# Kernel optimization log

Hardware: AMD Instinct MI355X
Metric: run time of the kernel (lower is better)

Reference implementation:

```python
import jax, jax.numpy as jnp
import numpy as np

B, Ng, C, H, W, Nt, M, P = 4, 8192, 256, 128, 128, 512, 8, 4
Ch = C // M  # 32 channels per head
EPS = 1e-5


def setup_inputs():
    key = jax.random.key(0)
    ks = jax.random.split(key, 12)
    s = 0.02
    def w(k, shape):
        return jax.random.normal(k, shape, jnp.float32) * s
    return {
        "query": jax.random.normal(ks[0], (B, Ng, C), jnp.float32),
        "value": jax.random.normal(ks[1], (B, C, H, W), jnp.float32),
        "reference_points": jax.random.uniform(ks[2], (B, Ng, 2), dtype=jnp.float32),
        "trajectory_points": jax.random.uniform(ks[3], (B, Nt, 2), dtype=jnp.float32),
        "in_proj_w": w(ks[4], (3 * C, C)),
        "in_proj_b": jnp.zeros((3 * C,), jnp.float32),
        "mha_out_w": w(ks[5], (C, C)),
        "mha_out_b": jnp.zeros((C,), jnp.float32),
        "ln_g": jnp.ones((C,), jnp.float32),
        "ln_b": jnp.zeros((C,), jnp.float32),
        "traj_w": w(ks[6], (C, 2)),
        "traj_b": jnp.zeros((C,), jnp.float32),
        "offs_w": w(ks[7], (M * P * 2, C)),
        "offs_b": jnp.zeros((M * P * 2,), jnp.float32),
        "attw_w": w(ks[8], (M * P, C)),
        "attw_b": jnp.zeros((M * P,), jnp.float32),
        "out_w": w(ks[9], (C, C)),
        "out_b": jnp.zeros((C,), jnp.float32),
    }


def _bilinear_sample(imgf, x, y):
    # imgf: (NM, Ch, H*W); x, y: (NM, Lq, P) unnormalized pixel coords
    # grid_sample semantics: bilinear, padding_mode='zeros', align_corners=False
    NM = imgf.shape[0]
    Lq, Pp = x.shape[1], x.shape[2]
    x0 = jnp.floor(x); y0 = jnp.floor(y)
    x1 = x0 + 1.0;     y1 = y0 + 1.0

    def gather(xi, yi):
        valid = (xi >= 0) & (xi < W) & (yi >= 0) & (yi < H)
        xc = jnp.clip(xi, 0, W - 1).astype(jnp.int32)
        yc = jnp.clip(yi, 0, H - 1).astype(jnp.int32)
        idx = (yc * W + xc).reshape(NM, 1, Lq * Pp)
        v = jnp.take_along_axis(imgf, jnp.broadcast_to(idx, (NM, Ch, Lq * Pp)), axis=2)
        return v.reshape(NM, Ch, Lq, Pp), valid.astype(imgf.dtype)

    v00, m00 = gather(x0, y0)
    v01, m01 = gather(x1, y0)
    v10, m10 = gather(x0, y1)
    v11, m11 = gather(x1, y1)
    wx1 = x - x0; wx0 = 1.0 - wx1
    wy1 = y - y0; wy0 = 1.0 - wy1
    out = (v00 * (wx0 * wy0 * m00)[:, None]
         + v01 * (wx1 * wy0 * m01)[:, None]
         + v10 * (wx0 * wy1 * m10)[:, None]
         + v11 * (wx1 * wy1 * m11)[:, None])
    return out  # (NM, Ch, Lq, P)


def reference(query, value, reference_points, trajectory_points,
              in_proj_w, in_proj_b, mha_out_w, mha_out_b, ln_g, ln_b,
              traj_w, traj_b, offs_w, offs_b, attw_w, attw_b, out_w, out_b):
    # trajectory projection: (B,Nt,2) -> (B,Nt,C)
    tf = trajectory_points @ traj_w.T + traj_b

    # guidance cross-attention (nn.MultiheadAttention, eval mode => no dropout)
    wq, wk, wv = jnp.split(in_proj_w, 3, axis=0)
    bq, bk, bv = jnp.split(in_proj_b, 3, axis=0)
    q = (query @ wq.T + bq).reshape(B, Ng, M, Ch)
    k = (tf @ wk.T + bk).reshape(B, Nt, M, Ch)
    v = (tf @ wv.T + bv).reshape(B, Nt, M, Ch)
    scores = jnp.einsum('bqmc,bkmc->bmqk', q, k) / jnp.sqrt(jnp.float32(Ch))
    probs = jax.nn.softmax(scores, axis=-1)
    ctx = jnp.einsum('bmqk,bkmc->bqmc', probs, v).reshape(B, Ng, C)
    ctx = ctx @ mha_out_w.T + mha_out_b

    # residual + LayerNorm
    x = query + ctx
    mu = x.mean(-1, keepdims=True)
    var = ((x - mu) ** 2).mean(-1, keepdims=True)
    gq = (x - mu) / jnp.sqrt(var + EPS) * ln_g + ln_b

    # sampling offsets & softmax attention weights (L=1 level)
    offs = (gq @ offs_w.T + offs_b).reshape(B, Ng, M, 1, P, 2)
    aw = jax.nn.softmax((gq @ attw_w.T + attw_b).reshape(B, Ng, M, P), axis=-1)
    loc = reference_points[:, :, None, None, None, :] + offs  # (B,Ng,M,1,P,2)

    # deformable sampling core (single level)
    grid = 2.0 * loc[:, :, :, 0] - 1.0                   # (B,Ng,M,P,2)
    grid = grid.transpose(0, 2, 1, 3, 4).reshape(B * M, Ng, P, 2)
    gx = (grid[..., 0] + 1.0) * (W * 0.5) - 0.5
    gy = (grid[..., 1] + 1.0) * (H * 0.5) - 0.5
    imgf = value.reshape(B * M, Ch, H * W)               # per-head feature maps
    samp = _bilinear_sample(imgf, gx, gy)                # (B*M,Ch,Ng,P)
    w_att = aw.transpose(0, 2, 1, 3).reshape(B * M, 1, Ng, P)
    out = (samp * w_att).sum(-1)                         # (B*M,Ch,Ng)

    # faithful to source: view(B,M,Ch,Ng).transpose(1,2).contiguous().view(B,Ng,C)
    out = out.reshape(B, M, Ch, Ng).transpose(0, 2, 1, 3).reshape(B, Ng, C)
    return out @ out_w.T + out_b
```

## Files before the change

### kernel.cpp

```cpp
#include <hip/hip_runtime.h>
#include <hip/hip_bf16.h>
#include <stdint.h>

typedef __bf16 bf16_t;
typedef __bf16 bf16x8 __attribute__((ext_vector_type(8)));
typedef __bf16 bf16x4 __attribute__((ext_vector_type(4)));
typedef float f32x4 __attribute__((ext_vector_type(4)));

#define CEXP 0.25506807186679906f

__device__ __forceinline__ float ldf(const void* p, size_t i, int isf) {
  return isf ? ((const float*)p)[i] : (float)((const bf16_t*)p)[i];
}

__device__ __forceinline__ int detect_isf(const void* q) {
  const uint16_t* u = (const uint16_t*)q;
  const int lane = threadIdx.x & 63;
  const uint16_t v = u[2 * lane];
  const int e = (v >> 7) & 0xFF;
  const int weird = (e >= 0x86 || (v != 0 && e <= 0x65)) ? 1 : 0;
  return (__popcll(__ballot(weird)) >= 16) ? 1 : 0;
}

__device__ __forceinline__ float fexp2(float x) {
#if __has_builtin(__builtin_amdgcn_exp2f)
  return __builtin_amdgcn_exp2f(x);
#else
  return exp2f(x);
#endif
}

__device__ __forceinline__ f32x4 mfma16x16x16(bf16x4 a, bf16x4 b, f32x4 c) {
#if __has_builtin(__builtin_amdgcn_mfma_f32_16x16x16_bf16)
  return __builtin_amdgcn_mfma_f32_16x16x16_bf16(a, b, c, 0, 0, 0);
#else
  typedef short s16x4 __attribute__((ext_vector_type(4)));
  return __builtin_amdgcn_mfma_f32_16x16x16bf16_1k(
      __builtin_bit_cast(s16x4, a), __builtin_bit_cast(s16x4, b), c, 0, 0, 0);
#endif
}

__device__ __forceinline__ void stage16(const bf16_t* g, bf16_t* l) {
  __builtin_amdgcn_global_load_lds((const __attribute__((address_space(1))) void*)g,
                                   (__attribute__((address_space(3))) void*)l, 16, 0, 0);
}

__global__ __launch_bounds__(256) void prep_all(
    const void* __restrict__ query,
    const void* in_w, const void* in_b, const void* mow, const void* mob,
    const void* outw, const void* outb,
    const void* trajp, const void* tw, const void* tb,
    const void* offs_w, const void* attw_w, const void* offs_b, const void* attw_b,
    bf16_t* __restrict__ blob, bf16_t* __restrict__ tf,
    bf16_t* __restrict__ Wph, bf16_t* __restrict__ Wpl, bf16_t* __restrict__ bp)
{
  const int isf = detect_isf(query);
  const int bid = blockIdx.x;
  if (bid < 322) {
    const int g = (bid * 256 + threadIdx.x) * 4;
    if (g >= 328960) return;
    const void* src; size_t off;
    if      (g < 196608) { src = in_w; off = g; }
    else if (g < 197376) { src = in_b; off = g - 196608; }
    else if (g < 262912) { src = mow;  off = g - 197376; }
    else if (g < 263168) { src = mob;  off = g - 262912; }
    else if (g < 328704) { src = outw; off = g - 263168; }
    else                 { src = outb; off = g - 328704; }
#pragma unroll
    for (int k = 0; k < 4; k++) blob[g + k] = (bf16_t)ldf(src, off + k, isf);
  } else if (bid < 322 + 2048) {
    const int rowb = bid - 322;
    const int c = threadIdx.x;
    const float x = ldf(trajp, rowb * 2 + 0, isf);
    const float y = ldf(trajp, rowb * 2 + 1, isf);
    const float v = x * ldf(tw, c * 2 + 0, isf) + y * ldf(tw, c * 2 + 1, isf) + ldf(tb, c, isf);
    tf[(size_t)rowb * 256 + c] = (bf16_t)v;
  } else {
    const int idx = (bid - 2370) * 256 + threadIdx.x;
    const int rowp = idx >> 8, c = idx & 255;
    float v = 0.0f;
    if (rowp < 64)      v = ldf(offs_w, rowp * 256 + c, isf);
    else if (rowp < 96) v = ldf(attw_w, (rowp - 64) * 256 + c, isf);
    const bf16_t hi = (bf16_t)v;
    Wph[idx] = hi;
    Wpl[idx] = (bf16_t)(v - (float)hi);
    if (idx < 128) {
      float bv = 0.0f;
      if (idx < 64)      bv = ldf(offs_b, idx, isf);
      else if (idx < 96) bv = ldf(attw_b, idx - 64, isf);
      bp[idx] = (bf16_t)bv;
    }
  }
}

#define TM 128
#define TN 128
#define TKK 64

__global__ __launch_bounds__(256) void gemm_async(
    const bf16_t* __restrict__ A, const bf16_t* __restrict__ W,
    const bf16_t* __restrict__ bias, void* __restrict__ Cout,
    void* __restrict__ Cout2, int Ndim, int Kdim, int mode, float kscale,
    const void* __restrict__ qdet)
{
  __shared__ __align__(16) bf16_t As[TM * TKK];
  __shared__ __align__(16) bf16_t Ws[TN * TKK];
  const int t    = threadIdx.x;
  const int lane = t & 63;
  const int w    = t >> 6;
  const int wm   = (w & 1) * 64;
  const int wn   = (w >> 1) * 64;
  const int q4   = lane >> 4;
  const int r16  = lane & 15;
  const int tm   = blockIdx.x * TM;
  const int tn   = blockIdx.y * TN;

  f32x4 acc[4][4] = {};

  for (int kt = 0; kt < Kdim; kt += TKK) {
    __syncthreads();
#pragma unroll
    for (int r = 0; r < 4; r++) {
      const int L = w * 256 + r * 64 + lane;
      const int R = L >> 3, c = (L & 7) * 8;
      stage16(A + (size_t)(tm + R) * Kdim + kt + c, As + L * 8);
      stage16(W + (size_t)(tn + R) * Kdim + kt + c, Ws + L * 8);
    }
    __syncthreads();
#pragma unroll
    for (int ks = 0; ks < TKK; ks += 32) {
      bf16x8 af[4], bfm[4];
#pragma unroll
      for (int i = 0; i < 4; i++)
        af[i] = *(const bf16x8*)(As + (wm + 16 * i + r16) * TKK + ks + q4 * 8);
#pragma unroll
      for (int j = 0; j < 4; j++)
        bfm[j] = *(const bf16x8*)(Ws + (wn + 16 * j + r16) * TKK + ks + q4 * 8);
#pragma unroll
      for (int i = 0; i < 4; i++)
#pragma unroll
        for (int j = 0; j < 4; j++)
          acc[i][j] = __builtin_amdgcn_mfma_f32_16x16x32_bf16(af[i], bfm[j], acc[i][j], 0, 0, 0);
    }
  }

  const int isf = (mode == 3) ? detect_isf(qdet) : 1;
#pragma unroll
  for (int j = 0; j < 4; j++) {
    const int col = tn + wn + 16 * j + r16;
    const float bv = (float)bias[col];
#pragma unroll
    for (int i = 0; i < 4; i++) {
      const int row0 = tm + wm + 16 * i + q4 * 4;
#pragma unroll
      for (int rr = 0; rr < 4; rr++) {
        const float v = acc[i][j][rr] + bv;
        const size_t off = (size_t)(row0 + rr) * Ndim + col;
        if (mode == 0) {
          ((bf16_t*)Cout)[off] = (bf16_t)v;
        } else if (mode == 6) {
          const int rowg = row0 + rr;
          if (col < 256) {
            ((bf16_t*)Cout)[(size_t)rowg * 256 + col] = (bf16_t)(v * kscale);
          } else {
            const int bb = rowg >> 9, tt = rowg & 511;
            const int c2 = col - 256;
            const int mm = c2 >> 5, ch = c2 & 31;
            ((bf16_t*)Cout2)[(((size_t)(bb * 8 + mm) * 32 + ch) << 9) + tt] = (bf16_t)v;
          }
        } else {
          if (isf) ((float*)Cout)[off] = v; else ((bf16_t*)Cout)[off] = (bf16_t)v;
        }
      }
    }
  }
}

__global__ __launch_bounds__(256) void gemm_f32a(
    const void* __restrict__ Araw, const bf16_t* __restrict__ W,
    const bf16_t* __restrict__ bias, bf16_t* __restrict__ Cout,
    int Ndim, int Kdim, const void* __restrict__ qdet)
{
  __shared__ __align__(16) bf16_t As[TM * TKK];
  __shared__ __align__(16) bf16_t Ws[TN * TKK];
  const int t    = threadIdx.x;
  const int lane = t & 63;
  const int w    = t >> 6;
  const int wm   = (w & 1) * 64;
  const int wn   = (w >> 1) * 64;
  const int q4   = lane >> 4;
  const int r16  = lane & 15;
  const int tm   = blockIdx.x * TM;
  const int tn   = blockIdx.y * TN;
  const int aisf = detect_isf(qdet);

  f32x4 acc[4][4] = {};
  const int srow = t >> 1;
  const int skb  = (t & 1) * 32;

  for (int kt = 0; kt < Kdim; kt += TKK) {
    __syncthreads();
    if (aisf) {
      const float4* ga = (const float4*)((const float*)Araw + (size_t)(tm + srow) * Kdim + kt + skb);
#pragma unroll
      for (int kk = 0; kk < 8; kk++) {
        const float4 u = ga[kk];
        bf16x4 h = {(bf16_t)u.x, (bf16_t)u.y, (bf16_t)u.z, (bf16_t)u.w};
        *(bf16x4*)(As + srow * TKK + skb + kk * 4) = h;
      }
    } else {
      const uint4* ga = (const uint4*)((const bf16_t*)Araw + (size_t)(tm + srow) * Kdim + kt + skb);
      uint4* la = (uint4*)(As + srow * TKK + skb);
      la[0] = ga[0]; la[1] = ga[1]; la[2] = ga[2]; la[3] = ga[3];
    }
    {
      const uint4* gw = (const uint4*)(W + (size_t)(tn + srow) * Kdim + kt + skb);
      uint4* lw = (uint4*)(Ws + srow * TKK + skb);
      lw[0] = gw[0]; lw[1] = gw[1]; lw[2] = gw[2]; lw[3] = gw[3];
    }
    __syncthreads();
#pragma unroll
    for (int ks = 0; ks < TKK; ks += 32) {
      bf16x8 af[4], bfm[4];
#pragma unroll
      for (int i = 0; i < 4; i++)
        af[i] = *(const bf16x8*)(As + (wm + 16 * i + r16) * TKK + ks + q4 * 8);
#pragma unroll
      for (int j = 0; j < 4; j++)
        bfm[j] = *(const bf16x8*)(Ws + (wn + 16 * j + r16) * TKK + ks + q4 * 8);
#pragma unroll
      for (int i = 0; i < 4; i++)
#pragma unroll
        for (int j = 0; j < 4; j++)
          acc[i][j] = __builtin_amdgcn_mfma_f32_16x16x32_bf16(af[i], bfm[j], acc[i][j], 0, 0, 0);
    }
  }

#pragma unroll
  for (int j = 0; j < 4; j++) {
    const int col = tn + wn + 16 * j + r16;
    const float bv = (float)bias[col];
#pragma unroll
    for (int i = 0; i < 4; i++) {
      const int row0 = tm + wm + 16 * i + q4 * 4;
#pragma unroll
      for (int rr = 0; rr < 4; rr++)
        Cout[(size_t)(row0 + rr) * Ndim + col] = (bf16_t)(acc[i][j][rr] + bv);
    }
  }
}

__global__ __launch_bounds__(256, 4) void attn_kernel(
    const bf16_t* __restrict__ Q, const bf16_t* __restrict__ Kk,
    const bf16_t* __restrict__ Vt, bf16_t* __restrict__ ctx)
{
  const int t = threadIdx.x;
  const int lane = t & 63, w = t >> 6;
  const int q4 = lane >> 4, r16 = lane & 15;
  const int bm = blockIdx.y;
  const int b = bm >> 3, m = bm & 7;
  const int q0 = blockIdx.x * 256 + w * 64;

  bf16x8 qf[4];
#pragma unroll
  for (int qt = 0; qt < 4; qt++)
    qf[qt] = *(const bf16x8*)(Q + ((size_t)(b * 8192 + q0 + qt * 16 + r16) * 256 + m * 32 + q4 * 8));

  f32x4 acc[4][2] = {};
  float lsum[4] = {0.f, 0.f, 0.f, 0.f};

  const bf16_t* kbase  = Kk + (size_t)b * 512 * 256 + m * 32 + (size_t)r16 * 256 + q4 * 8;
  const bf16_t* vbase0 = Vt + (size_t)bm * 32 * 512 + ((size_t)r16 << 9) + q4 * 4;
  const bf16_t* vbase1 = vbase0 + (16 << 9);

  bf16x8 kf = *(const bf16x8*)(kbase);
  bf16x4 v0 = *(const bf16x4*)(vbase0);
  bf16x4 v1 = *(const bf16x4*)(vbase1);

  for (int k0 = 0; k0 < 512; k0 += 16) {
    const int nxt = k0 + 16;
    const bf16x8 kf_n = *(const bf16x8*)(kbase + (size_t)nxt * 256);
    const bf16x4 v0_n = *(const bf16x4*)(vbase0 + nxt);
    const bf16x4 v1_n = *(const bf16x4*)(vbase1 + nxt);
#pragma unroll
    for (int qt = 0; qt < 4; qt++) {
      f32x4 z = {};
      const f32x4 s = __builtin_amdgcn_mfma_f32_16x16x32_bf16(kf, qf[qt], z, 0, 0, 0);
      const float e0 = fexp2(s[0]), e1 = fexp2(s[1]);
      const float e2 = fexp2(s[2]), e3 = fexp2(s[3]);
      lsum[qt] += (e0 + e1) + (e2 + e3);
      const bf16x4 p = {(bf16_t)e0, (bf16_t)e1, (bf16_t)e2, (bf16_t)e3};
      acc[qt][0] = mfma16x16x16(v0, p, acc[qt][0]);
      acc[qt][1] = mfma16x16x16(v1, p, acc[qt][1]);
    }
    kf = kf_n; v0 = v0_n; v1 = v1_n;
  }

#pragma unroll
  for (int qt = 0; qt < 4; qt++) {
    float v = lsum[qt];
    v += __shfl_xor(v, 16, 64);
    v += __shfl_xor(v, 32, 64);
    const float inv = 1.0f / v;
    const size_t row = (size_t)b * 8192 + q0 + qt * 16 + r16;
    bf16x4 o0, o1;
#pragma unroll
    for (int rr = 0; rr < 4; rr++) {
      o0[rr] = (bf16_t)(acc[qt][0][rr] * inv);
      o1[rr] = (bf16_t)(acc[qt][1][rr] * inv);
    }
    *(bf16x4*)(ctx + row * 256 + m * 32 + q4 * 4)      = o0;
    *(bf16x4*)(ctx + row * 256 + m * 32 + 16 + q4 * 4) = o1;
  }
}

__global__ __launch_bounds__(256) void ln_kernel(
    const bf16_t* __restrict__ y2, const void* __restrict__ query,
    const void* __restrict__ g, const void* __restrict__ beta,
    bf16_t* __restrict__ gqh, bf16_t* __restrict__ gql)
{
  const int isf = detect_isf(query);
  const int rowb = blockIdx.x * 4 + (threadIdx.x >> 6);
  const int lane = threadIdx.x & 63;
  const size_t base = (size_t)rowb * 256;
  const int c0 = lane * 4;
  float x[4];
  {
    const bf16x4 yv = *(const bf16x4*)(y2 + base + c0);
    if (isf) {
      const float4 qv = *(const float4*)((const float*)query + base + c0);
      x[0] = qv.x + (float)yv[0]; x[1] = qv.y + (float)yv[1];
      x[2] = qv.z + (float)yv[2]; x[3] = qv.w + (float)yv[3];
    } else {
      const bf16x4 qv = *(const bf16x4*)((const bf16_t*)query + base + c0);
#pragma unroll
      for (int k = 0; k < 4; k++) x[k] = (float)qv[k] + (float)yv[k];
    }
  }
  float s = x[0] + x[1] + x[2] + x[3];
  for (int d = 1; d < 64; d <<= 1) s += __shfl_xor(s, d, 64);
  const float mu = s * (1.0f / 256.0f);
  float vs = 0.f;
#pragma unroll
  for (int k = 0; k < 4; k++) { const float d = x[k] - mu; vs += d * d; }
  for (int d = 1; d < 64; d <<= 1) vs += __shfl_xor(vs, d, 64);
  const float rstd = rsqrtf(vs * (1.0f / 256.0f) + 1e-5f);
  float gw[4], bb[4];
  if (isf) {
    const float4 gg = *(const float4*)((const float*)g + c0);
    const float4 bv = *(const float4*)((const float*)beta + c0);
    gw[0] = gg.x; gw[1] = gg.y; gw[2] = gg.z; gw[3] = gg.w;
    bb[0] = bv.x; bb[1] = bv.y; bb[2] = bv.z; bb[3] = bv.w;
  } else {
    const bf16x4 gg = *(const bf16x4*)((const bf16_t*)g + c0);
    const bf16x4 bv = *(const bf16x4*)((const bf16_t*)beta + c0);
#pragma unroll
    for (int k = 0; k < 4; k++) { gw[k] = (float)gg[k]; bb[k] = (float)bv[k]; }
  }
  bf16x4 hi4, lo4;
#pragma unroll
  for (int k = 0; k < 4; k++) {
    const float gv = (x[k] - mu) * rstd * gw[k] + bb[k];
    const bf16_t hi = (bf16_t)gv;
    hi4[k] = hi;
    lo4[k] = (bf16_t)(gv - (float)hi);
  }
  *(bf16x4*)(gqh + base + c0) = hi4;
  *(bf16x4*)(gql + base + c0) = lo4;
}

__global__ __launch_bounds__(256) void gemm_offs(
    const bf16_t* __restrict__ Ahg, const bf16_t* __restrict__ Alg,
    const bf16_t* __restrict__ Whg, const bf16_t* __restrict__ Wlg,
    const bf16_t* __restrict__ bias, float* __restrict__ Cout)
{
  __shared__ __align__(16) bf16_t Ah[128 * 64];
  __shared__ __align__(16) bf16_t Al[128 * 64];
  __shared__ __align__(16) bf16_t Wh[128 * 64];
  __shared__ __align__(16) bf16_t Wl[128 * 64];
  const int t    = threadIdx.x;
  const int lane = t & 63;
  const int w    = t >> 6;
  const int wm   = (w & 1) * 64;
  const int wn   = (w >> 1) * 64;
  const int q4   = lane >> 4;
  const int r16  = lane & 15;
  const int tm   = blockIdx.x * 128;

  f32x4 acc[4][4] = {};
  const int srow = t >> 1;
  const int skb  = (t & 1) * 32;

  for (int kt = 0; kt < 256; kt += 64) {
    __syncthreads();
    {
      const uint4* g0 = (const uint4*)(Ahg + (size_t)(tm + srow) * 256 + kt + skb);
      uint4* l0 = (uint4*)(Ah + srow * 64 + skb);
      l0[0] = g0[0]; l0[1] = g0[1]; l0[2] = g0[2]; l0[3] = g0[3];
      const uint4* g1 = (const uint4*)(Alg + (size_t)(tm + srow) * 256 + kt + skb);
      uint4* l1 = (uint4*)(Al + srow * 64 + skb);
      l1[0] = g1[0]; l1[1] = g1[1]; l1[2] = g1[2]; l1[3] = g1[3];
      const uint4* g2 = (const uint4*)(Whg + (size_t)srow * 256 + kt + skb);
      uint4* l2 = (uint4*)(Wh + srow * 64 + skb);
      l2[0] = g2[0]; l2[1] = g2[1]; l2[2] = g2[2]; l2[3] = g2[3];
      const uint4* g3 = (const uint4*)(Wlg + (size_t)srow * 256 + kt + skb);
      uint4* l3 = (uint4*)(Wl + srow * 64 + skb);
      l3[0] = g3[0]; l3[1] = g3[1]; l3[2] = g3[2]; l3[3] = g3[3];
    }
    __syncthreads();
#pragma unroll
    for (int ks = 0; ks < 64; ks += 32) {
      bf16x8 ah[4], al[4], bh[4], bl[4];
#pragma unroll
      for (int i = 0; i < 4; i++) {
        ah[i] = *(const bf16x8*)(Ah + (wm + 16 * i + r16) * 64 + ks + q4 * 8);
        al[i] = *(const bf16x8*)(Al + (wm + 16 * i + r16) * 64 + ks + q4 * 8);
      }
#pragma unroll
      for (int j = 0; j < 4; j++) {
        bh[j] = *(const bf16x8*)(Wh + (wn + 16 * j + r16) * 64 + ks + q4 * 8);
        bl[j] = *(const bf16x8*)(Wl + (wn + 16 * j + r16) * 64 + ks + q4 * 8);
      }
#pragma unroll
      for (int i = 0; i < 4; i++)
#pragma unroll
        for (int j = 0; j < 4; j++) {
          f32x4 a = acc[i][j];
          a = __builtin_amdgcn_mfma_f32_16x16x32_bf16(al[i], bh[j], a, 0, 0, 0);
          a = __builtin_amdgcn_mfma_f32_16x16x32_bf16(ah[i], bl[j], a, 0, 0, 0);
          a = __builtin_amdgcn_mfma_f32_16x16x32_bf16(ah[i], bh[j], a, 0, 0, 0);
          acc[i][j] = a;
        }
    }
  }

#pragma unroll
  for (int j = 0; j < 4; j++) {
    const int col = wn + 16 * j + r16;
    const float bv = (float)bias[col];
#pragma unroll
    for (int i = 0; i < 4; i++) {
      const int row0 = tm + wm + 16 * i + q4 * 4;
#pragma unroll
      for (int rr = 0; rr < 4; rr++)
        Cout[(size_t)(row0 + rr) * 128 + col] = acc[i][j][rr] + bv;
    }
  }
}

__global__ __launch_bounds__(256) void transpose_value(
    const void* __restrict__ V, bf16_t* __restrict__ Vp, const void* __restrict__ qdet)
{
  __shared__ __align__(16) bf16_t tile[32][136];
  const int isf = detect_isf(qdet);
  const int bid = blockIdx.x;
  const int h = bid & 127;
  const int bm = bid >> 7;
  const int b = bm >> 3, mm = bm & 7;
  const int t = threadIdx.x;
  const int ch  = t >> 3;
  const int ww0 = (t & 7) * 16;
  const size_t ibase = (((size_t)b * 256 + mm * 32 + ch) * 128 + h) * 128 + ww0;
  if (isf) {
    const float4* src = (const float4*)((const float*)V + ibase);
    bf16x8 h0, h1;
#pragma unroll
    for (int k = 0; k < 2; k++) {
      const float4 u0 = src[k * 2], u1 = src[k * 2 + 1];
      bf16x8 hh = {(bf16_t)u0.x, (bf16_t)u0.y, (bf16_t)u0.z, (bf16_t)u0.w,
                   (bf16_t)u1.x, (bf16_t)u1.y, (bf16_t)u1.z, (bf16_t)u1.w};
      if (k == 0) h0 = hh; else h1 = hh;
    }
    *(bf16x8*)(&tile[ch][ww0])     = h0;
    *(bf16x8*)(&tile[ch][ww0 + 8]) = h1;
  } else {
    const bf16x8* src = (const bf16x8*)((const bf16_t*)V + ibase);
    *(bf16x8*)(&tile[ch][ww0])     = src[0];
    *(bf16x8*)(&tile[ch][ww0 + 8]) = src[1];
  }
  __syncthreads();
  const size_t base = ((size_t)bm * 128 + h) * 4096;
  const int ww = t >> 1;
  const int c0 = (t & 1) * 16;
  bf16x8 o0, o1;
#pragma unroll
  for (int e = 0; e < 8; e++) { o0[e] = tile[c0 + e][ww]; o1[e] = tile[c0 + 8 + e][ww]; }
  *(bf16x8*)(Vp + base + ww * 32 + c0)     = o0;
  *(bf16x8*)(Vp + base + ww * 32 + c0 + 8) = o1;
}

__global__ __launch_bounds__(256) void sampler(
    const float* __restrict__ ys, const void* __restrict__ refp,
    const bf16_t* __restrict__ vperm, bf16_t* __restrict__ outs,
    const void* __restrict__ qdet)
{
  const int isf = detect_isf(qdet);
  const int t = threadIdx.x;
  const int qt = blockIdx.x;
  const int bm = blockIdx.y;
  const int b = bm >> 3, m = bm & 7;
  const int qq = qt * 256 + t;
  const size_t row = (size_t)b * 8192 + qq;
  const float* y = ys + row * 128;
  const float rx = ldf(refp, row * 2 + 0, isf);
  const float ry = ldf(refp, row * 2 + 1, isf);

  const float l0 = y[64 + m * 4 + 0], l1 = y[64 + m * 4 + 1];
  const float l2 = y[64 + m * 4 + 2], l3 = y[64 + m * 4 + 3];
  const float mx = fmaxf(fmaxf(l0, l1), fmaxf(l2, l3));
  const float e0 = __expf(l0 - mx), e1 = __expf(l1 - mx);
  const float e2 = __expf(l2 - mx), e3 = __expf(l3 - mx);
  const float inv = 1.0f / (e0 + e1 + e2 + e3);
  const float aw[4] = {e0 * inv, e1 * inv, e2 * inv, e3 * inv};

  float acc[32];
#pragma unroll
  for (int ch = 0; ch < 32; ch++) acc[ch] = 0.0f;

  const bf16_t* vbase = vperm + (size_t)bm * (128 * 128 * 32);

  for (int p = 0; p < 4; p++) {
    const float gx = (rx + y[m * 8 + p * 2 + 0]) * 128.0f - 0.5f;
    const float gy = (ry + y[m * 8 + p * 2 + 1]) * 128.0f - 0.5f;
    const float x0f = floorf(gx), y0f = floorf(gy);
    const int x0 = (int)x0f, y0i = (int)y0f;
    const float wx1 = gx - x0f, wx0 = 1.0f - wx1;
    const float wy1 = gy - y0f, wy0 = 1.0f - wy1;
    const float a = aw[p];
    for (int cy = 0; cy < 2; cy++) {
      const int yy = y0i + cy;
      if (yy < 0 || yy >= 128) continue;
      const float wy = cy ? wy1 : wy0;
      for (int cx = 0; cx < 2; cx++) {
        const int xx = x0 + cx;
        if (xx < 0 || xx >= 128) continue;
        const float wgt = a * wy * (cx ? wx1 : wx0);
        const bf16x8* src8 = (const bf16x8*)(vbase + ((size_t)yy * 128 + xx) * 32);
#pragma unroll
        for (int vv = 0; vv < 4; vv++) {
          const bf16x8 d = src8[vv];
#pragma unroll
          for (int e = 0; e < 8; e++) acc[vv * 8 + e] += wgt * (float)d[e];
        }
      }
    }
  }

  const size_t obase = (size_t)b * 8192;
#pragma unroll
  for (int ch = 0; ch < 32; ch++) {
    const size_t orow = obase + (size_t)(ch * 8 + m) * 32 + qt;
    outs[orow * 256 + t] = (bf16_t)acc[ch];
  }
}

extern "C" void kernel_launch(void* const* d_in, const int* in_sizes, int n_in,
                              void* d_out, int out_size, void* d_ws, size_t ws_size,
                              hipStream_t stream) {
  const void* query = d_in[0];
  const void* value = d_in[1];
  const void* refp  = d_in[2];
  const void* trajp = d_in[3];
  const void* in_w  = d_in[4];
  const void* in_b  = d_in[5];
  const void* mow   = d_in[6];
  const void* mob   = d_in[7];
  const void* lng   = d_in[8];
  const void* lnb   = d_in[9];
  const void* tw    = d_in[10];
  const void* tb    = d_in[11];
  const void* ow    = d_in[12];
  const void* ob    = d_in[13];
  const void* aww   = d_in[14];
  const void* awb   = d_in[15];
  const void* outw  = d_in[16];
  const void* outb  = d_in[17];

  char* base = (char*)d_ws;
  float*  ysamp = (float*)(base);
  bf16_t* qout  = (bf16_t*)(base + 16777216);
  bf16_t* ctx   = (bf16_t*)(base + 33554432);
  bf16_t* y2    = (bf16_t*)(base + 50331648);
  bf16_t* tf_ws = (bf16_t*)(base + 67108864);
  bf16_t* k_ws  = (bf16_t*)(base + 68157440);
  bf16_t* vt_g  = (bf16_t*)(base + 69206016);
  bf16_t* blob  = (bf16_t*)(base + 70254592);

  bf16_t* gqh   = qout;
  bf16_t* gql   = ctx;
  bf16_t* vperm = (bf16_t*)(base + 16777216);
  bf16_t* outs  = y2;

  bf16_t* inw_bf  = blob;
  bf16_t* inb_bf  = blob + 196608;
  bf16_t* mow_bf  = blob + 197376;
  bf16_t* mob_bf  = blob + 262912;
  bf16_t* outw_bf = blob + 263168;
  bf16_t* outb_bf = blob + 328704;
  bf16_t* wph     = blob + 328960;
  bf16_t* wpl     = blob + 361728;
  bf16_t* bpad    = blob + 394496;

  prep_all<<<dim3(2498), dim3(256), 0, stream>>>(
      query, in_w, in_b, mow, mob, outw, outb, trajp, tw, tb,
      ow, aww, ob, awb, blob, tf_ws, wph, wpl, bpad);
  gemm_async<<<dim3(16, 4), dim3(256), 0, stream>>>(
      tf_ws, inw_bf + 65536, inb_bf + 256, (void*)k_ws, (void*)vt_g, 512, 256, 6, CEXP, query);
  gemm_f32a<<<dim3(256, 2), dim3(256), 0, stream>>>(
      query, inw_bf, inb_bf, qout, 256, 256, query);
  attn_kernel<<<dim3(32, 32), dim3(256), 0, stream>>>(qout, k_ws, vt_g, ctx);
  gemm_async<<<dim3(256, 2), dim3(256), 0, stream>>>(
      ctx, mow_bf, mob_bf, (void*)y2, nullptr, 256, 256, 0, 1.0f, query);
  ln_kernel<<<dim3(8192), dim3(256), 0, stream>>>(y2, query, lng, lnb, gqh, gql);
  gemm_offs<<<dim3(256, 1), dim3(256), 0, stream>>>(gqh, gql, wph, wpl, bpad, ysamp);
  transpose_value<<<dim3(4096), dim3(256), 0, stream>>>(value, vperm, query);
  sampler<<<dim3(32, 32), dim3(256), 0, stream>>>(ysamp, refp, vperm, outs, query);
  gemm_async<<<dim3(256, 2), dim3(256), 0, stream>>>(
      outs, outw_bf, outb_bf, d_out, nullptr, 256, 256, 3, 1.0f, query);
}
```

Baseline: 360.5 us.

## Double query tiles per wave in attention and double-buffer K/V loads

Each attention wave now handles 128 queries (8 tiles) instead of 64, so every K/V fragment loaded is reused across twice as many query tiles. The key loop is unrolled by two with A/B register prefetch buffers two steps ahead, and s_setprio raises wave priority around the MFMA/exp blocks. The grid is halved and launch bounds drop to 2 blocks per SM to allow the extra registers, which lowers occupancy and leaves fewer blocks to cover the GPU. On the final iteration the prefetch reads past key 512 into the neighbouring K/V data, as the old code already did, but the values are never used.

```diff
diff --git a/kernel.cpp b/kernel.cpp
--- a/kernel.cpp
+++ b/kernel.cpp
@@ -250,7 +250,7 @@
   }
 }
 
-__global__ __launch_bounds__(256, 4) void attn_kernel(
+__global__ __launch_bounds__(256, 2) void attn_kernel(
     const bf16_t* __restrict__ Q, const bf16_t* __restrict__ Kk,
     const bf16_t* __restrict__ Vt, bf16_t* __restrict__ ctx)
 {
@@ -259,45 +259,68 @@
   const int q4 = lane >> 4, r16 = lane & 15;
   const int bm = blockIdx.y;
   const int b = bm >> 3, m = bm & 7;
-  const int q0 = blockIdx.x * 256 + w * 64;
-
-  bf16x8 qf[4];
-#pragma unroll
-  for (int qt = 0; qt < 4; qt++)
+  const int q0 = blockIdx.x * 512 + w * 128;
+
+  bf16x8 qf[8];
+#pragma unroll
+  for (int qt = 0; qt < 8; qt++)
     qf[qt] = *(const bf16x8*)(Q + ((size_t)(b * 8192 + q0 + qt * 16 + r16) * 256 + m * 32 + q4 * 8));
 
-  f32x4 acc[4][2] = {};
-  float lsum[4] = {0.f, 0.f, 0.f, 0.f};
+  f32x4 acc[8][2] = {};
+  float lsum[8] = {0.f, 0.f, 0.f, 0.f, 0.f, 0.f, 0.f, 0.f};
 
   const bf16_t* kbase  = Kk + (size_t)b * 512 * 256 + m * 32 + (size_t)r16 * 256 + q4 * 8;
   const bf16_t* vbase0 = Vt + (size_t)bm * 32 * 512 + ((size_t)r16 << 9) + q4 * 4;
   const bf16_t* vbase1 = vbase0 + (16 << 9);
 
-  bf16x8 kf = *(const bf16x8*)(kbase);
-  bf16x4 v0 = *(const bf16x4*)(vbase0);
-  bf16x4 v1 = *(const bf16x4*)(vbase1);
-
-  for (int k0 = 0; k0 < 512; k0 += 16) {
-    const int nxt = k0 + 16;
-    const bf16x8 kf_n = *(const bf16x8*)(kbase + (size_t)nxt * 256);
-    const bf16x4 v0_n = *(const bf16x4*)(vbase0 + nxt);
-    const bf16x4 v1_n = *(const bf16x4*)(vbase1 + nxt);
-#pragma unroll
-    for (int qt = 0; qt < 4; qt++) {
+  bf16x8 kfA = *(const bf16x8*)(kbase);
+  bf16x4 v0A = *(const bf16x4*)(vbase0);
+  bf16x4 v1A = *(const bf16x4*)(vbase1);
+  bf16x8 kfB = *(const bf16x8*)(kbase + (size_t)16 * 256);
+  bf16x4 v0B = *(const bf16x4*)(vbase0 + 16);
+  bf16x4 v1B = *(const bf16x4*)(vbase1 + 16);
+
+  for (int k0 = 0; k0 < 512; k0 += 32) {
+    const bf16x8 ka = kfA;
+    const bf16x4 va0 = v0A, va1 = v1A;
+    kfA = *(const bf16x8*)(kbase + (size_t)(k0 + 32) * 256);
+    v0A = *(const bf16x4*)(vbase0 + k0 + 32);
+    v1A = *(const bf16x4*)(vbase1 + k0 + 32);
+    __builtin_amdgcn_s_setprio(1);
+#pragma unroll
+    for (int qt = 0; qt < 8; qt++) {
       f32x4 z = {};
-      const f32x4 s = __builtin_amdgcn_mfma_f32_16x16x32_bf16(kf, qf[qt], z, 0, 0, 0);
+      const f32x4 s = __builtin_amdgcn_mfma_f32_16x16x32_bf16(ka, qf[qt], z, 0, 0, 0);
       const float e0 = fexp2(s[0]), e1 = fexp2(s[1]);
       const float e2 = fexp2(s[2]), e3 = fexp2(s[3]);
       lsum[qt] += (e0 + e1) + (e2 + e3);
       const bf16x4 p = {(bf16_t)e0, (bf16_t)e1, (bf16_t)e2, (bf16_t)e3};
-      acc[qt][0] = mfma16x16x16(v0, p, acc[qt][0]);
-      acc[qt][1] = mfma16x16x16(v1, p, acc[qt][1]);
-    }
-    kf = kf_n; v0 = v0_n; v1 = v1_n;
-  }
-
-#pragma unroll
-  for (int qt = 0; qt < 4; qt++) {
+      acc[qt][0] = mfma16x16x16(va0, p, acc[qt][0]);
+      acc[qt][1] = mfma16x16x16(va1, p, acc[qt][1]);
+    }
+    __builtin_amdgcn_s_setprio(0);
+    const bf16x8 kb = kfB;
+    const bf16x4 vb0 = v0B, vb1 = v1B;
+    kfB = *(const bf16x8*)(kbase + (size_t)(k0 + 48) * 256);
+    v0B = *(const bf16x4*)(vbase0 + k0 + 48);
+    v1B = *(const bf16x4*)(vbase1 + k0 + 48);
+    __builtin_amdgcn_s_setprio(1);
+#pragma unroll
+    for (int qt = 0; qt < 8; qt++) {
+      f32x4 z = {};
+      const f32x4 s = __builtin_amdgcn_mfma_f32_16x16x32_bf16(kb, qf[qt], z, 0, 0, 0);
+      const float e0 = fexp2(s[0]), e1 = fexp2(s[1]);
+      const float e2 = fexp2(s[2]), e3 = fexp2(s[3]);
+      lsum[qt] += (e0 + e1) + (e2 + e3);
+      const bf16x4 p = {(bf16_t)e0, (bf16_t)e1, (bf16_t)e2, (bf16_t)e3};
+      acc[qt][0] = mfma16x16x16(vb0, p, acc[qt][0]);
+      acc[qt][1] = mfma16x16x16(vb1, p, acc[qt][1]);
+    }
+    __builtin_amdgcn_s_setprio(0);
+  }
+
+#pragma unroll
+  for (int qt = 0; qt < 8; qt++) {
     float v = lsum[qt];
     v += __shfl_xor(v, 16, 64);
     v += __shfl_xor(v, 32, 64);
@@ -608,7 +631,7 @@
       tf_ws, inw_bf + 65536, inb_bf + 256, (void*)k_ws, (void*)vt_g, 512, 256, 6, CEXP, query);
   gemm_f32a<<<dim3(256, 2), dim3(256), 0, stream>>>(
       query, inw_bf, inb_bf, qout, 256, 256, query);
-  attn_kernel<<<dim3(32, 32), dim3(256), 0, stream>>>(qout, k_ws, vt_g, ctx);
+  attn_kernel<<<dim3(16, 32), dim3(256), 0, stream>>>(qout, k_ws, vt_g, ctx);
   gemm_async<<<dim3(256, 2), dim3(256), 0, stream>>>(
       ctx, mow_bf, mob_bf, (void*)y2, nullptr, 256, 256, 0, 1.0f, query);
   ln_kernel<<<dim3(8192), dim3(256), 0, stream>>>(y2, query, lng, lnb, gqh, gql);
```

Result: faster. 342.0 us (-5.1%).
